# Performance work log

Hardware: AMD Instinct MI355X
Metric: run time of the kernel (lower is better)

Reference implementation:

```python
import jax, jax.numpy as jnp
import numpy as np

B_, T_, D_ = 8, 4096, 1024  # batch, seq_len, input_dim == state_dim


def setup_inputs() -> dict:
    key = jax.random.key(0)
    ks = jax.random.split(key, 9)
    s = 1.0 / np.sqrt(D_)  # nn.Linear default init scale
    return {
        "u":   jax.random.normal(ks[0], (B_, T_, D_), dtype=jnp.float32),
        "WA":  jax.random.uniform(ks[1], (D_, D_), jnp.float32, -s, s),
        "WB":  jax.random.uniform(ks[2], (D_, D_), jnp.float32, -s, s),
        "WAf": jax.random.uniform(ks[3], (D_, D_), jnp.float32, -s, s),
        "WBf": jax.random.uniform(ks[4], (D_, D_), jnp.float32, -s, s),
        "w1":  jax.random.uniform(ks[5], (1, D_), jnp.float32, -s, s),
        "w2":  jax.random.uniform(ks[6], (1, D_), jnp.float32, -s, s),
        "b":   jnp.zeros((1,), dtype=jnp.float32),
        "Wc":  jax.random.uniform(ks[7], (1, D_), jnp.float32, -s, s),
    }


def reference(u, WA, WB, WAf, WBf, w1, w2, b, Wc):
    # NOTE: the torch loop reads x_forward/x_backward from the pre-loop zeros
    # tensor, so A(.)/Af(.) are always applied to zeros. Actual math:
    #   x_f[0] = u[0];      x_f[t]   = B  u[t]    for t >= 1
    #   x_b[T-1] = u[T-1];  x_b[t]   = Bf u[t+1]  for t <= T-2
    bsz, seq_len, _ = u.shape
    xf = jnp.concatenate([u[:, :1], jnp.einsum('btd,ed->bte', u[:, 1:], WB)], axis=1)
    xb = jnp.concatenate([jnp.einsum('btd,ed->bte', u[:, 1:], WBf), u[:, -1:]], axis=1)
    gamma = jax.nn.sigmoid(xf @ w1.T + xb @ w2.T + b)       # (b, t, 1)
    y = gamma * (xf + xb) + (1.0 - gamma) * u               # (b, t, d)
    final_output = jax.nn.sigmoid(y @ Wc.T).reshape(bsz, seq_len)
    return y, gamma, final_output
```

## Files before the change

kernel.cpp:

```cpp
#include <hip/hip_runtime.h>
#include <hip/hip_bf16.h>
#include <cstddef>

#define GLOBAL_AS __attribute__((address_space(1)))
#define LDS_AS __attribute__((address_space(3)))

typedef __bf16 bf16_t;
typedef __bf16 bf16x8 __attribute__((ext_vector_type(8)));
typedef __bf16 bf16x4 __attribute__((ext_vector_type(4)));
typedef float f32x4 __attribute__((ext_vector_type(4)));

static constexpr int Tseq  = 4096;
static constexpr int Dd    = 1024;
static constexpr int Mrows = 8 * 4096;
static constexpr int Ncat  = 2048;

__global__ __launch_bounds__(256) void k_cast_u(const float* __restrict__ src,
                                                bf16_t* __restrict__ dst) {
    const int i = blockIdx.x * 256 + threadIdx.x;
    float4 v = reinterpret_cast<const float4*>(src)[i];
    bf16x4 o;
    o[0] = (__bf16)v.x; o[1] = (__bf16)v.y; o[2] = (__bf16)v.z; o[3] = (__bf16)v.w;
    reinterpret_cast<bf16x4*>(dst)[i] = o;
}

__global__ __launch_bounds__(256) void k_cast_w(const float* __restrict__ WB,
                                                const float* __restrict__ WBf,
                                                bf16_t* __restrict__ dst) {
    const int i  = blockIdx.x * 256 + threadIdx.x;
    const int e4 = i * 4;
    const float* s = (e4 < 1024 * 1024) ? (WB + e4) : (WBf + (e4 - 1024 * 1024));
    float4 v = *reinterpret_cast<const float4*>(s);
    bf16x4 o;
    o[0] = (__bf16)v.x; o[1] = (__bf16)v.y; o[2] = (__bf16)v.z; o[3] = (__bf16)v.w;
    reinterpret_cast<bf16x4*>(dst)[i] = o;
}

__global__ __launch_bounds__(256, 2) void k_gemm(const bf16_t* __restrict__ A,
                                                 const bf16_t* __restrict__ Bt,
                                                 bf16_t* __restrict__ xf,
                                                 bf16_t* __restrict__ xb) {
    __shared__ bf16_t As[128 * 64];
    __shared__ bf16_t Bs[128 * 64];

    const int bid  = blockIdx.x;
    const int bcol = bid & 15;
    const int brow = bid >> 4;
    const int tid  = threadIdx.x;
    const int wid  = tid >> 6;
    const int lane = tid & 63;
    const int wr = wid >> 1, wc = wid & 1;
    const int lane15 = lane & 15;
    const int laneK  = (lane >> 4) * 8;

    f32x4 acc[4][4] = {};

    const size_t aRow0 = (size_t)brow * 128;
    const size_t bRow0 = (size_t)bcol * 128;

    for (int k0 = 0; k0 < 1024; k0 += 64) {
        if (k0) __syncthreads();
        #pragma unroll
        for (int it = 0; it < 4; ++it) {
            const int l   = (wid * 4 + it) * 512 + lane * 8;
            const int row = l >> 6;
            const int col = l & 63;
            const bf16_t* ga = A  + (aRow0 + row) * 1024 + k0 + col;
            const bf16_t* gb = Bt + (bRow0 + row) * 1024 + k0 + col;
            __builtin_amdgcn_global_load_lds((const GLOBAL_AS void*)ga,
                (LDS_AS void*)(As + (wid * 4 + it) * 512), 16, 0, 0);
            __builtin_amdgcn_global_load_lds((const GLOBAL_AS void*)gb,
                (LDS_AS void*)(Bs + (wid * 4 + it) * 512), 16, 0, 0);
        }
        __syncthreads();

        #pragma unroll
        for (int kk = 0; kk < 2; ++kk) {
            bf16x8 af[4], bfv[4];
            #pragma unroll
            for (int m = 0; m < 4; ++m)
                af[m] = *reinterpret_cast<const bf16x8*>(
                    As + (wr * 64 + m * 16 + lane15) * 64 + kk * 32 + laneK);
            #pragma unroll
            for (int n = 0; n < 4; ++n)
                bfv[n] = *reinterpret_cast<const bf16x8*>(
                    Bs + (wc * 64 + n * 16 + lane15) * 64 + kk * 32 + laneK);
            #pragma unroll
            for (int m = 0; m < 4; ++m)
                #pragma unroll
                for (int n = 0; n < 4; ++n)
                    acc[m][n] = __builtin_amdgcn_mfma_f32_16x16x32_bf16(
                        af[m], bfv[n], acc[m][n], 0, 0, 0);
        }
    }

    const bool isF  = (bcol < 8);
    const int rbase = brow * 128 + wr * 64 + (lane >> 4) * 4;
    const int cbase = (isF ? bcol : bcol - 8) * 128 + wc * 64 + lane15;
    #pragma unroll
    for (int m = 0; m < 4; ++m) {
        #pragma unroll
        for (int j = 0; j < 4; ++j) {
            const int r = rbase + m * 16 + j;
            #pragma unroll
            for (int n = 0; n < 4; ++n) {
                const int c = cbase + n * 16;
                const __bf16 v = (__bf16)acc[m][n][j];
                if (isF)           xf[(size_t)r * 1024 + c]       = v;
                else if (r >= 1)   xb[(size_t)(r - 1) * 1024 + c] = v;
            }
        }
    }
}

__global__ __launch_bounds__(256) void k_epi(const float* __restrict__ u,
                                             const bf16_t* __restrict__ xf,
                                             const bf16_t* __restrict__ xb,
                                             const float* __restrict__ w1,
                                             const float* __restrict__ w2,
                                             const float* __restrict__ bb,
                                             const float* __restrict__ Wc,
                                             float* __restrict__ y,
                                             float* __restrict__ gout,
                                             float* __restrict__ fout) {
    const int m   = blockIdx.x;
    const int t   = m & (Tseq - 1);
    const int tid = threadIdx.x;
    const int j0  = tid * 4;
    const size_t rb = (size_t)m * Dd;

    const float4 uu = *reinterpret_cast<const float4*>(u + rb + j0);

    float xfl[4], xbl[4];
    if (t == 0) {
        xfl[0] = uu.x; xfl[1] = uu.y; xfl[2] = uu.z; xfl[3] = uu.w;
    } else {
        bf16x4 v = *reinterpret_cast<const bf16x4*>(xf + rb + j0);
        #pragma unroll
        for (int j = 0; j < 4; ++j) xfl[j] = (float)v[j];
    }
    if (t == Tseq - 1) {
        xbl[0] = uu.x; xbl[1] = uu.y; xbl[2] = uu.z; xbl[3] = uu.w;
    } else {
        bf16x4 v = *reinterpret_cast<const bf16x4*>(xb + rb + j0);
        #pragma unroll
        for (int j = 0; j < 4; ++j) xbl[j] = (float)v[j];
    }

    const float4 w1v = *reinterpret_cast<const float4*>(w1 + j0);
    const float4 w2v = *reinterpret_cast<const float4*>(w2 + j0);

    float part = xfl[0] * w1v.x + xfl[1] * w1v.y + xfl[2] * w1v.z + xfl[3] * w1v.w
               + xbl[0] * w2v.x + xbl[1] * w2v.y + xbl[2] * w2v.z + xbl[3] * w2v.w;
    #pragma unroll
    for (int off = 32; off >= 1; off >>= 1) part += __shfl_xor(part, off);

    __shared__ float red1[4];
    __shared__ float red2[4];
    if ((tid & 63) == 0) red1[tid >> 6] = part;
    __syncthreads();
    const float logit = red1[0] + red1[1] + red1[2] + red1[3] + bb[0];
    const float g = 1.0f / (1.0f + __expf(-logit));

    float4 yv;
    yv.x = g * (xfl[0] + xbl[0]) + (1.0f - g) * uu.x;
    yv.y = g * (xfl[1] + xbl[1]) + (1.0f - g) * uu.y;
    yv.z = g * (xfl[2] + xbl[2]) + (1.0f - g) * uu.z;
    yv.w = g * (xfl[3] + xbl[3]) + (1.0f - g) * uu.w;
    *reinterpret_cast<float4*>(y + rb + j0) = yv;

    const float4 wcv = *reinterpret_cast<const float4*>(Wc + j0);
    float p2 = yv.x * wcv.x + yv.y * wcv.y + yv.z * wcv.z + yv.w * wcv.w;
    #pragma unroll
    for (int off = 32; off >= 1; off >>= 1) p2 += __shfl_xor(p2, off);
    if ((tid & 63) == 0) red2[tid >> 6] = p2;
    __syncthreads();
    if (tid == 0) {
        const float fl = red2[0] + red2[1] + red2[2] + red2[3];
        gout[m] = g;
        fout[m] = 1.0f / (1.0f + __expf(-fl));
    }
}

extern "C" void kernel_launch(void* const* d_in, const int* in_sizes, int n_in,
                              void* d_out, int out_size, void* d_ws, size_t ws_size,
                              hipStream_t stream) {
    const float* u   = (const float*)d_in[0];
    const float* WB  = (const float*)d_in[2];
    const float* WBf = (const float*)d_in[4];
    const float* w1  = (const float*)d_in[5];
    const float* w2  = (const float*)d_in[6];
    const float* bb  = (const float*)d_in[7];
    const float* Wc  = (const float*)d_in[8];

    char* ws = (char*)d_ws;
    bf16_t* u16  = (bf16_t*)(ws);
    bf16_t* wcat = (bf16_t*)(ws + 67108864);
    bf16_t* xfw  = (bf16_t*)(ws + 71303168);
    bf16_t* xbw  = (bf16_t*)(ws + 138412032);

    float* y    = (float*)d_out;
    float* gout = y + (size_t)Mrows * Dd;
    float* fout = gout + Mrows;

    k_cast_u<<<dim3(32768), dim3(256), 0, stream>>>(u, u16);
    k_cast_w<<<dim3(2048),  dim3(256), 0, stream>>>(WB, WBf, wcat);

    k_gemm<<<dim3(4096), dim3(256), 0, stream>>>(u16, wcat, xfw, xbw);

    k_epi<<<dim3(Mrows), dim3(256), 0, stream>>>(u, xfw, xbw, w1, w2, bb, Wc,
                                                 y, gout, fout);
}
```

Before: 466.6 us.

## Rewrite GEMM as 256x256 double-buffered pipelined tiles and wave-per-row epilogue

The GEMM moves from 128x128 tiles with 4 waves to 256x256 tiles with 8 waves. It adds double-buffered LDS staged through global_load_lds, an XOR-swizzled LDS layout, block-index swizzling for L2 locality, and interleaved quarter-tile MFMA phases with manual vmcnt waits, barriers and setprio. The aim is to hide global load latency behind MFMA work and raise arithmetic intensity. The epilogue now gives each wave one row, so the cross-wave LDS reductions and __syncthreads disappear. The risks are the 128KB LDS footprint limiting occupancy and the fragile hand-tuned waitcnt sequencing.

Result: faster. 444.9 us (-4.6%).

```diff
diff --git a/kernel.cpp b/kernel.cpp
--- a/kernel.cpp
+++ b/kernel.cpp
@@ -13,7 +13,6 @@
 static constexpr int Tseq  = 4096;
 static constexpr int Dd    = 1024;
 static constexpr int Mrows = 8 * 4096;
-static constexpr int Ncat  = 2048;
 
 __global__ __launch_bounds__(256) void k_cast_u(const float* __restrict__ src,
                                                 bf16_t* __restrict__ dst) {
@@ -36,81 +35,138 @@
     reinterpret_cast<bf16x4*>(dst)[i] = o;
 }
 
-__global__ __launch_bounds__(256, 2) void k_gemm(const bf16_t* __restrict__ A,
+__global__ __launch_bounds__(512, 2) void k_gemm(const bf16_t* __restrict__ A,
                                                  const bf16_t* __restrict__ Bt,
                                                  bf16_t* __restrict__ xf,
                                                  bf16_t* __restrict__ xb) {
-    __shared__ bf16_t As[128 * 64];
-    __shared__ bf16_t Bs[128 * 64];
-
-    const int bid  = blockIdx.x;
-    const int bcol = bid & 15;
-    const int brow = bid >> 4;
+    __shared__ __align__(16) char sm[131072];
+
     const int tid  = threadIdx.x;
     const int wid  = tid >> 6;
     const int lane = tid & 63;
-    const int wr = wid >> 1, wc = wid & 1;
     const int lane15 = lane & 15;
-    const int laneK  = (lane >> 4) * 8;
-
-    f32x4 acc[4][4] = {};
-
-    const size_t aRow0 = (size_t)brow * 128;
-    const size_t bRow0 = (size_t)bcol * 128;
-
-    for (int k0 = 0; k0 < 1024; k0 += 64) {
-        if (k0) __syncthreads();
-        #pragma unroll
-        for (int it = 0; it < 4; ++it) {
-            const int l   = (wid * 4 + it) * 512 + lane * 8;
-            const int row = l >> 6;
-            const int col = l & 63;
-            const bf16_t* ga = A  + (aRow0 + row) * 1024 + k0 + col;
-            const bf16_t* gb = Bt + (bRow0 + row) * 1024 + k0 + col;
-            __builtin_amdgcn_global_load_lds((const GLOBAL_AS void*)ga,
-                (LDS_AS void*)(As + (wid * 4 + it) * 512), 16, 0, 0);
-            __builtin_amdgcn_global_load_lds((const GLOBAL_AS void*)gb,
-                (LDS_AS void*)(Bs + (wid * 4 + it) * 512), 16, 0, 0);
+    const int g16  = (lane >> 4) * 16;
+    const int wmq  = wid >> 1;
+    const int wnq  = wid & 1;
+
+    const int bid0 = blockIdx.x;
+    const int swzb = (bid0 & 7) * 128 + (bid0 >> 3);
+    const int bcol = swzb & 7;
+    const int brow = swzb >> 3;
+
+    const int srow = tid >> 3;
+    const int scol = ((tid & 7) ^ (srow & 7)) * 8;
+    const bf16_t* gA = A  + ((size_t)brow * 256 + srow) * 1024 + scol;
+    const bf16_t* gB = Bt + ((size_t)bcol * 256 + srow) * 1024 + scol;
+
+    char* const smw = sm + wid * 1024;
+
+    f32x4 acc[2][2][2][4] = {};
+    bf16x8 afr[2][2], bfr[4][2];
+
+#define STAGE(bufb, isA, h, kt1) do {                                          \
+    const bf16_t* _s = ((isA) ? gA : gB) + (size_t)(h) * 131072 + (kt1) * 64;  \
+    char* _l = smw + (bufb) * 65536 + ((isA) ? 0 : 32768) + (h) * 16384;       \
+    __builtin_amdgcn_global_load_lds((const GLOBAL_AS void*)_s,                \
+                                     (LDS_AS void*)_l, 16, 0, 0);              \
+    __builtin_amdgcn_global_load_lds((const GLOBAL_AS void*)(_s + 65536),      \
+                                     (LDS_AS void*)(_l + 8192), 16, 0, 0);     \
+} while (0)
+
+#define RD_A(bufb, mhh) do {                                                   \
+    _Pragma("unroll") for (int mi = 0; mi < 2; ++mi) {                         \
+      const int rr = wmq * 32 + mi * 16 + lane15;                              \
+      const char* _p = sm + (bufb) * 65536 + (mhh) * 16384 + rr * 128;         \
+      const int sz = (rr & 7) << 4;                                            \
+      _Pragma("unroll") for (int kk = 0; kk < 2; ++kk)                         \
+        afr[mi][kk] = *reinterpret_cast<const bf16x8*>(_p + ((kk * 64 + g16) ^ sz)); \
+    } } while (0)
+
+#define RD_B(bufb, nhh) do {                                                   \
+    _Pragma("unroll") for (int ni = 0; ni < 4; ++ni) {                         \
+      const int rr = wnq * 64 + ni * 16 + lane15;                              \
+      const char* _p = sm + (bufb) * 65536 + 32768 + (nhh) * 16384 + rr * 128; \
+      const int sz = (rr & 7) << 4;                                            \
+      _Pragma("unroll") for (int kk = 0; kk < 2; ++kk)                         \
+        bfr[ni][kk] = *reinterpret_cast<const bf16x8*>(_p + ((kk * 64 + g16) ^ sz)); \
+    } } while (0)
+
+#define MM(MH, NH) do {                                                        \
+    __builtin_amdgcn_s_setprio(1);                                             \
+    _Pragma("unroll") for (int kk = 0; kk < 2; ++kk)                           \
+    _Pragma("unroll") for (int mi = 0; mi < 2; ++mi)                           \
+    _Pragma("unroll") for (int ni = 0; ni < 4; ++ni)                           \
+      acc[MH][mi][NH][ni] = __builtin_amdgcn_mfma_f32_16x16x32_bf16(           \
+          afr[mi][kk], bfr[ni][kk], acc[MH][mi][NH][ni], 0, 0, 0);             \
+    __builtin_amdgcn_s_setprio(0);                                             \
+} while (0)
+
+#define BARM() asm volatile("s_barrier" ::: "memory")
+
+    STAGE(0, 1, 0, 0);
+    STAGE(0, 0, 0, 0);
+    STAGE(0, 1, 1, 0);
+    STAGE(0, 0, 1, 0);
+    asm volatile("s_waitcnt vmcnt(4)" ::: "memory");
+    BARM();
+
+#pragma unroll 2
+    for (int t = 0; t < 16; ++t) {
+        const int buf = t & 1;
+        const bool pf = t < 15;
+        const int k1 = t + 1;
+        RD_A(buf, 0); RD_B(buf, 0);
+        if (pf) STAGE(buf ^ 1, 1, 0, k1);
+        __builtin_amdgcn_s_barrier();
+        MM(0, 0);
+        if (pf) { asm volatile("s_waitcnt vmcnt(4)" ::: "memory"); }
+        else    { asm volatile("s_waitcnt vmcnt(2)" ::: "memory"); }
+        BARM();
+        RD_A(buf, 1);
+        if (pf) STAGE(buf ^ 1, 0, 0, k1);
+        __builtin_amdgcn_s_barrier();
+        MM(1, 0);
+        if (pf) { asm volatile("s_waitcnt vmcnt(4)" ::: "memory"); }
+        else    { asm volatile("s_waitcnt vmcnt(0)" ::: "memory"); }
+        BARM();
+        RD_B(buf, 1);
+        if (pf) STAGE(buf ^ 1, 1, 1, k1);
+        __builtin_amdgcn_s_barrier();
+        MM(1, 1);
+        BARM();
+        RD_A(buf, 0);
+        if (pf) STAGE(buf ^ 1, 0, 1, k1);
+        __builtin_amdgcn_s_barrier();
+        MM(0, 1);
+        if (pf) { asm volatile("s_waitcnt vmcnt(4)" ::: "memory"); }
+        BARM();
+    }
+
+    const bool isF  = bcol < 4;
+    const int rbase = brow * 256 + wmq * 32 + (lane >> 4) * 4;
+    const int cb0   = bcol * 256 + wnq * 64 + lane15;
+    #pragma unroll
+    for (int mh = 0; mh < 2; ++mh)
+    #pragma unroll
+    for (int mi = 0; mi < 2; ++mi)
+    #pragma unroll
+    for (int j = 0; j < 4; ++j) {
+        const int r = rbase + mh * 128 + mi * 16 + j;
+        #pragma unroll
+        for (int nh = 0; nh < 2; ++nh)
+        #pragma unroll
+        for (int ni = 0; ni < 4; ++ni) {
+            const int c = cb0 + nh * 128 + ni * 16;
+            const __bf16 v = (__bf16)acc[mh][mi][nh][ni][j];
+            if (isF)         xf[(size_t)r * 1024 + c] = v;
+            else if (r >= 1) xb[(size_t)(r - 1) * 1024 + (c - 1024)] = v;
         }
-        __syncthreads();
-
-        #pragma unroll
-        for (int kk = 0; kk < 2; ++kk) {
-            bf16x8 af[4], bfv[4];
-            #pragma unroll
-            for (int m = 0; m < 4; ++m)
-                af[m] = *reinterpret_cast<const bf16x8*>(
-                    As + (wr * 64 + m * 16 + lane15) * 64 + kk * 32 + laneK);
-            #pragma unroll
-            for (int n = 0; n < 4; ++n)
-                bfv[n] = *reinterpret_cast<const bf16x8*>(
-                    Bs + (wc * 64 + n * 16 + lane15) * 64 + kk * 32 + laneK);
-            #pragma unroll
-            for (int m = 0; m < 4; ++m)
-                #pragma unroll
-                for (int n = 0; n < 4; ++n)
-                    acc[m][n] = __builtin_amdgcn_mfma_f32_16x16x32_bf16(
-                        af[m], bfv[n], acc[m][n], 0, 0, 0);
-        }
-    }
-
-    const bool isF  = (bcol < 8);
-    const int rbase = brow * 128 + wr * 64 + (lane >> 4) * 4;
-    const int cbase = (isF ? bcol : bcol - 8) * 128 + wc * 64 + lane15;
-    #pragma unroll
-    for (int m = 0; m < 4; ++m) {
-        #pragma unroll
-        for (int j = 0; j < 4; ++j) {
-            const int r = rbase + m * 16 + j;
-            #pragma unroll
-            for (int n = 0; n < 4; ++n) {
-                const int c = cbase + n * 16;
-                const __bf16 v = (__bf16)acc[m][n][j];
-                if (isF)           xf[(size_t)r * 1024 + c]       = v;
-                else if (r >= 1)   xb[(size_t)(r - 1) * 1024 + c] = v;
-            }
-        }
-    }
+    }
+#undef STAGE
+#undef RD_A
+#undef RD_B
+#undef MM
+#undef BARM
 }
 
 __global__ __launch_bounds__(256) void k_epi(const float* __restrict__ u,
@@ -123,62 +179,75 @@
                                              float* __restrict__ y,
                                              float* __restrict__ gout,
                                              float* __restrict__ fout) {
-    const int m   = blockIdx.x;
-    const int t   = m & (Tseq - 1);
-    const int tid = threadIdx.x;
-    const int j0  = tid * 4;
-    const size_t rb = (size_t)m * Dd;
-
-    const float4 uu = *reinterpret_cast<const float4*>(u + rb + j0);
-
-    float xfl[4], xbl[4];
+    const int lane = threadIdx.x & 63;
+    const int row  = blockIdx.x * 4 + (threadIdx.x >> 6);
+    const int t    = row & (Tseq - 1);
+    const size_t rb = (size_t)row * Dd;
+
+    float uv[16], xfv[16], xbv[16];
+    #pragma unroll
+    for (int j = 0; j < 2; ++j) {
+        const int e = j * 512 + lane * 8;
+        const float4 u0 = *reinterpret_cast<const float4*>(u + rb + e);
+        const float4 u1 = *reinterpret_cast<const float4*>(u + rb + e + 4);
+        uv[j*8+0] = u0.x; uv[j*8+1] = u0.y; uv[j*8+2] = u0.z; uv[j*8+3] = u0.w;
+        uv[j*8+4] = u1.x; uv[j*8+5] = u1.y; uv[j*8+6] = u1.z; uv[j*8+7] = u1.w;
+        const bf16x8 f8 = *reinterpret_cast<const bf16x8*>(xf + rb + e);
+        const bf16x8 b8 = *reinterpret_cast<const bf16x8*>(xb + rb + e);
+        #pragma unroll
+        for (int i = 0; i < 8; ++i) { xfv[j*8+i] = (float)f8[i]; xbv[j*8+i] = (float)b8[i]; }
+    }
     if (t == 0) {
-        xfl[0] = uu.x; xfl[1] = uu.y; xfl[2] = uu.z; xfl[3] = uu.w;
-    } else {
-        bf16x4 v = *reinterpret_cast<const bf16x4*>(xf + rb + j0);
-        #pragma unroll
-        for (int j = 0; j < 4; ++j) xfl[j] = (float)v[j];
+        #pragma unroll
+        for (int i = 0; i < 16; ++i) xfv[i] = uv[i];
     }
     if (t == Tseq - 1) {
-        xbl[0] = uu.x; xbl[1] = uu.y; xbl[2] = uu.z; xbl[3] = uu.w;
-    } else {
-        bf16x4 v = *reinterpret_cast<const bf16x4*>(xb + rb + j0);
-        #pragma unroll
-        for (int j = 0; j < 4; ++j) xbl[j] = (float)v[j];
-    }
-
-    const float4 w1v = *reinterpret_cast<const float4*>(w1 + j0);
-    const float4 w2v = *reinterpret_cast<const float4*>(w2 + j0);
-
-    float part = xfl[0] * w1v.x + xfl[1] * w1v.y + xfl[2] * w1v.z + xfl[3] * w1v.w
-               + xbl[0] * w2v.x + xbl[1] * w2v.y + xbl[2] * w2v.z + xbl[3] * w2v.w;
+        #pragma unroll
+        for (int i = 0; i < 16; ++i) xbv[i] = uv[i];
+    }
+
+    float part = 0.0f;
+    #pragma unroll
+    for (int j = 0; j < 2; ++j) {
+        const int e = j * 512 + lane * 8;
+        const float4 a0 = *reinterpret_cast<const float4*>(w1 + e);
+        const float4 a1 = *reinterpret_cast<const float4*>(w1 + e + 4);
+        const float4 c0 = *reinterpret_cast<const float4*>(w2 + e);
+        const float4 c1 = *reinterpret_cast<const float4*>(w2 + e + 4);
+        part += xfv[j*8+0]*a0.x + xfv[j*8+1]*a0.y + xfv[j*8+2]*a0.z + xfv[j*8+3]*a0.w
+              + xfv[j*8+4]*a1.x + xfv[j*8+5]*a1.y + xfv[j*8+6]*a1.z + xfv[j*8+7]*a1.w
+              + xbv[j*8+0]*c0.x + xbv[j*8+1]*c0.y + xbv[j*8+2]*c0.z + xbv[j*8+3]*c0.w
+              + xbv[j*8+4]*c1.x + xbv[j*8+5]*c1.y + xbv[j*8+6]*c1.z + xbv[j*8+7]*c1.w;
+    }
     #pragma unroll
     for (int off = 32; off >= 1; off >>= 1) part += __shfl_xor(part, off);
-
-    __shared__ float red1[4];
-    __shared__ float red2[4];
-    if ((tid & 63) == 0) red1[tid >> 6] = part;
-    __syncthreads();
-    const float logit = red1[0] + red1[1] + red1[2] + red1[3] + bb[0];
-    const float g = 1.0f / (1.0f + __expf(-logit));
-
-    float4 yv;
-    yv.x = g * (xfl[0] + xbl[0]) + (1.0f - g) * uu.x;
-    yv.y = g * (xfl[1] + xbl[1]) + (1.0f - g) * uu.y;
-    yv.z = g * (xfl[2] + xbl[2]) + (1.0f - g) * uu.z;
-    yv.w = g * (xfl[3] + xbl[3]) + (1.0f - g) * uu.w;
-    *reinterpret_cast<float4*>(y + rb + j0) = yv;
-
-    const float4 wcv = *reinterpret_cast<const float4*>(Wc + j0);
-    float p2 = yv.x * wcv.x + yv.y * wcv.y + yv.z * wcv.z + yv.w * wcv.w;
+    const float g = 1.0f / (1.0f + __expf(-(part + bb[0])));
+
+    float p2 = 0.0f;
+    #pragma unroll
+    for (int j = 0; j < 2; ++j) {
+        const int e = j * 512 + lane * 8;
+        float4 y0, y1;
+        y0.x = g * (xfv[j*8+0] + xbv[j*8+0]) + (1.0f - g) * uv[j*8+0];
+        y0.y = g * (xfv[j*8+1] + xbv[j*8+1]) + (1.0f - g) * uv[j*8+1];
+        y0.z = g * (xfv[j*8+2] + xbv[j*8+2]) + (1.0f - g) * uv[j*8+2];
+        y0.w = g * (xfv[j*8+3] + xbv[j*8+3]) + (1.0f - g) * uv[j*8+3];
+        y1.x = g * (xfv[j*8+4] + xbv[j*8+4]) + (1.0f - g) * uv[j*8+4];
+        y1.y = g * (xfv[j*8+5] + xbv[j*8+5]) + (1.0f - g) * uv[j*8+5];
+        y1.z = g * (xfv[j*8+6] + xbv[j*8+6]) + (1.0f - g) * uv[j*8+6];
+        y1.w = g * (xfv[j*8+7] + xbv[j*8+7]) + (1.0f - g) * uv[j*8+7];
+        *reinterpret_cast<float4*>(y + rb + e)     = y0;
+        *reinterpret_cast<float4*>(y + rb + e + 4) = y1;
+        const float4 wc0 = *reinterpret_cast<const float4*>(Wc + e);
+        const float4 wc1 = *reinterpret_cast<const float4*>(Wc + e + 4);
+        p2 += y0.x*wc0.x + y0.y*wc0.y + y0.z*wc0.z + y0.w*wc0.w
+            + y1.x*wc1.x + y1.y*wc1.y + y1.z*wc1.z + y1.w*wc1.w;
+    }
     #pragma unroll
     for (int off = 32; off >= 1; off >>= 1) p2 += __shfl_xor(p2, off);
-    if ((tid & 63) == 0) red2[tid >> 6] = p2;
-    __syncthreads();
-    if (tid == 0) {
-        const float fl = red2[0] + red2[1] + red2[2] + red2[3];
-        gout[m] = g;
-        fout[m] = 1.0f / (1.0f + __expf(-fl));
+    if (lane == 0) {
+        gout[row] = g;
+        fout[row] = 1.0f / (1.0f + __expf(-p2));
     }
 }
 
@@ -206,8 +275,8 @@
     k_cast_u<<<dim3(32768), dim3(256), 0, stream>>>(u, u16);
     k_cast_w<<<dim3(2048),  dim3(256), 0, stream>>>(WB, WBf, wcat);
 
-    k_gemm<<<dim3(4096), dim3(256), 0, stream>>>(u16, wcat, xfw, xbw);
-
-    k_epi<<<dim3(Mrows), dim3(256), 0, stream>>>(u, xfw, xbw, w1, w2, bb, Wc,
-                                                 y, gout, fout);
-}
+    k_gemm<<<dim3(1024), dim3(512), 0, stream>>>(u16, wcat, xfw, xbw);
+
+    k_epi<<<dim3(Mrows / 4), dim3(256), 0, stream>>>(u, xfw, xbw, w1, w2, bb, Wc,
+                                                     y, gout, fout);
+}
```
